# Kernel tuning notes

Measured on AMD Instinct MI355X. Metric: run time of the kernel, lower is better.

## Reference

```python
import jax, jax.numpy as jnp
import numpy as np

L = 10      # num_mp_layers
N = 10000   # nodes
E = 160000  # edges (avg degree 16)
H = 128     # hidden_dim

def setup_inputs() -> dict:
    key = jax.random.key(0)
    ks = list(jax.random.split(key, 32))
    it = iter(ks)
    def nrm(shape, scale=0.05):
        return jax.random.normal(next(it), shape, dtype=jnp.float32) * scale
    inp = {
        'x': jax.random.normal(next(it), (N, 7), dtype=jnp.float32),
        'edge_index': jax.random.randint(next(it), (2, E), 0, N),
        'edge_attr': jax.random.normal(next(it), (E, 8), dtype=jnp.float32),
        # encoder: Linear(7,H) + LayerNorm(H) (+GELU)
        'enc_W': nrm((7, H)), 'enc_b': jnp.zeros((H,), jnp.float32),
        'enc_g': jnp.ones((H,), jnp.float32), 'enc_beta': jnp.zeros((H,), jnp.float32),
        # edge encoder: Linear(8,H)
        'eenc_W': nrm((8, H)), 'eenc_b': jnp.zeros((H,), jnp.float32),
        # per-layer edge MLP: Linear(3H,2H)+LN+GELU+Linear(2H,H)+LN (stacked over L)
        'eW1': nrm((L, 3 * H, 2 * H)), 'eb1': jnp.zeros((L, 2 * H), jnp.float32),
        'eg1': jnp.ones((L, 2 * H), jnp.float32), 'ebt1': jnp.zeros((L, 2 * H), jnp.float32),
        'eW2': nrm((L, 2 * H, H)), 'eb2': jnp.zeros((L, H), jnp.float32),
        'eg2': jnp.ones((L, H), jnp.float32), 'ebt2': jnp.zeros((L, H), jnp.float32),
        # per-layer node MLP: Linear(2H,2H)+LN+GELU+Linear(2H,H)+LN (stacked over L)
        'nW1': nrm((L, 2 * H, 2 * H)), 'nb1': jnp.zeros((L, 2 * H), jnp.float32),
        'ng1': jnp.ones((L, 2 * H), jnp.float32), 'nbt1': jnp.zeros((L, 2 * H), jnp.float32),
        'nW2': nrm((L, 2 * H, H)), 'nb2': jnp.zeros((L, H), jnp.float32),
        'ng2': jnp.ones((L, H), jnp.float32), 'nbt2': jnp.zeros((L, H), jnp.float32),
        # decoder: Linear(H,H)+GELU+Linear(H,4)
        'dW1': nrm((H, H)), 'db1': jnp.zeros((H,), jnp.float32),
        'dW2': nrm((H, 4)), 'db2': jnp.zeros((4,), jnp.float32),
    }
    return inp

def _ln(h, g, b):
    m = jnp.mean(h, axis=-1, keepdims=True)
    v = jnp.var(h, axis=-1, keepdims=True)  # biased, matches torch LayerNorm
    return (h - m) * jax.lax.rsqrt(v + 1e-5) * g + b

def _mlp(h, W1, b1, g1, bt1, W2, b2, g2, bt2):
    # Linear -> LayerNorm -> GELU (exact erf) -> [Dropout=eval noop] -> Linear -> LayerNorm
    h = jax.nn.gelu(_ln(h @ W1 + b1, g1, bt1), approximate=False)
    return _ln(h @ W2 + b2, g2, bt2)

def reference(x, edge_index, edge_attr,
              enc_W, enc_b, enc_g, enc_beta, eenc_W, eenc_b,
              eW1, eb1, eg1, ebt1, eW2, eb2, eg2, ebt2,
              nW1, nb1, ng1, nbt1, nW2, nb2, ng2, nbt2,
              dW1, db1, dW2, db2):
    row, col = edge_index[0], edge_index[1]
    n_nodes = x.shape[0]
    h = jax.nn.gelu(_ln(x @ enc_W + enc_b, enc_g, enc_beta), approximate=False)  # [N,H]
    e = edge_attr @ eenc_W + eenc_b                                              # [E,H]

    def step(carry, p):
        h, e = carry
        (w1, b1, g1, bt1, w2, b2, g2, bt2,
         v1, c1, m1, mt1, v2, c2, m2, mt2) = p
        # edge update: gather -> concat -> MLP -> residual
        edge_in = jnp.concatenate([h[row], h[col], e], axis=1)       # [E,3H]
        e = e + _mlp(edge_in, w1, b1, g1, bt1, w2, b2, g2, bt2)
        # scatter-mean aggregation onto destination (col) nodes
        agg = jax.ops.segment_sum(e, col, num_segments=n_nodes)      # [N,H]
        cnt = jax.ops.segment_sum(jnp.ones((e.shape[0], 1), e.dtype), col,
                                  num_segments=n_nodes)
        agg = agg / jnp.maximum(cnt, 1.0)
        # node update: concat -> MLP -> residual
        node_in = jnp.concatenate([h, agg], axis=1)                  # [N,2H]
        h = h + _mlp(node_in, v1, c1, m1, mt1, v2, c2, m2, mt2)
        return (h, e), None

    layer_params = (eW1, eb1, eg1, ebt1, eW2, eb2, eg2, ebt2,
                    nW1, nb1, ng1, nbt1, nW2, nb2, ng2, nbt2)
    (h, e), _ = jax.lax.scan(step, (h, e), layer_params)
    out = jax.nn.gelu(h @ dW1 + db1, approximate=False) @ dW2 + db2  # [N,4]
    return out
```

## Files before the change

kernel.cpp:

```cpp
#include <hip/hip_runtime.h>

#define L_LAYERS 10
#define NN 10000
#define EE 160000

typedef unsigned short ushort_t;
typedef unsigned int uint_t;
typedef __attribute__((ext_vector_type(8))) short bf16x8;
typedef __attribute__((ext_vector_type(4))) float floatx4;

__device__ __forceinline__ ushort_t f2b(float f) {
  uint_t u = __float_as_uint(f);
  u += 0x7FFFu + ((u >> 16) & 1u);
  return (ushort_t)(u >> 16);
}
__device__ __forceinline__ float b2f(ushort_t v) {
  return __uint_as_float(((uint_t)v) << 16);
}
__device__ __forceinline__ uint_t pk2(float lo, float hi) {
  uint_t ul = __float_as_uint(lo), uh = __float_as_uint(hi);
  ul += 0x7FFFu + ((ul >> 16) & 1u);
  uh += 0x7FFFu + ((uh >> 16) & 1u);
  return (ul >> 16) | (uh & 0xFFFF0000u);
}
__device__ __forceinline__ float gelu_exact(float x) {
  return 0.5f * x * (1.0f + erff(x * 0.7071067811865475f));
}
__device__ __forceinline__ float gelu_fast(float x) {
  float x2 = x * x;
  float inner = fmaf(0.044715f * x2, x, x);
  float E = __expf(-1.5957691216f * inner);
  float R = __builtin_amdgcn_rcpf(1.0f + E);
  return x * R;
}
template <int CTRL>
__device__ __forceinline__ float dpp_addf(float x) {
  int y = __builtin_amdgcn_update_dpp(0, __float_as_int(x), CTRL, 0xF, 0xF, true);
  return x + __int_as_float(y);
}
__device__ __forceinline__ float row16_sum(float x) {
  x = dpp_addf<0xB1>(x);
  x = dpp_addf<0x4E>(x);
  x = dpp_addf<0x141>(x);
  x = dpp_addf<0x140>(x);
  return x;
}
#define MFMA16x32(a, b, c) __builtin_amdgcn_mfma_f32_16x16x32_bf16((a), (b), (c), 0, 0, 0)

__global__ __launch_bounds__(256) void k_pack_w(
    const float* __restrict__ W, ushort_t* __restrict__ P, int K, int N, int LKN)
{
  int idx = blockIdx.x * 256 + threadIdx.x;
  if (idx >= LKN) return;
  int n = idx % N;
  int t = idx / N;
  int k = t % K;
  int l = t / K;
  int ks = k >> 5, kk = k & 31;
  int Ks = K >> 5;
  P[(((size_t)((l * Ks + ks) * N + n)) << 5) + kk] = f2b(W[idx]);
}

__global__ __launch_bounds__(128) void k_encoder(
    const float* __restrict__ x, const float* __restrict__ W,
    const float* __restrict__ b, const float* __restrict__ g,
    const float* __restrict__ bt, float* __restrict__ h, ushort_t* __restrict__ h_bf)
{
  const int n = blockIdx.x;
  const int j = threadIdx.x;
  __shared__ float xs[7];
  __shared__ float red[4];
  if (j < 7) xs[j] = x[n * 7 + j];
  __syncthreads();
  float z = b[j];
  #pragma unroll
  for (int k = 0; k < 7; ++k) z = fmaf(xs[k], W[k * 128 + j], z);
  float sm = z, sq = z * z;
  #pragma unroll
  for (int off = 32; off > 0; off >>= 1) {
    sm += __shfl_down(sm, off);
    sq += __shfl_down(sq, off);
  }
  const int wv = j >> 6, ln = j & 63;
  if (ln == 0) { red[wv] = sm; red[2 + wv] = sq; }
  __syncthreads();
  float m = (red[0] + red[1]) * (1.0f / 128.0f);
  float var = (red[2] + red[3]) * (1.0f / 128.0f) - m * m;
  float zz = (z - m) * rsqrtf(var + 1e-5f) * g[j] + bt[j];
  float o = gelu_exact(zz);
  h[(size_t)n * 128 + j] = o;
  h_bf[(size_t)n * 128 + j] = f2b(o);
}

__global__ __launch_bounds__(256) void k_edge_enc(
    const float* __restrict__ ea, const float* __restrict__ W,
    const float* __restrict__ b, ushort_t* __restrict__ e_bf)
{
  const int i = blockIdx.x * 256 + threadIdx.x;
  const int eid = i >> 7, j = i & 127;
  float z = b[j];
  #pragma unroll
  for (int k = 0; k < 8; ++k) z = fmaf(ea[eid * 8 + k], W[k * 128 + j], z);
  e_bf[i] = f2b(z);
}

__global__ void k_zero_cnt(int* __restrict__ cnt) {
  int i = blockIdx.x * 256 + threadIdx.x;
  if (i < NN) cnt[i] = 0;
}
__global__ void k_count(const int* __restrict__ eidx, int* __restrict__ cnt) {
  int i = blockIdx.x * 256 + threadIdx.x;
  atomicAdd(&cnt[eidx[EE + i]], 1);
}
__global__ __launch_bounds__(256) void k_scan(
    const int* __restrict__ cnt, int* __restrict__ rowptr, int* __restrict__ fillp)
{
  __shared__ int tot[256];
  __shared__ int off[257];
  const int t = threadIdx.x;
  const int C = 40;
  int s = 0;
  int lo = t * C, hi = lo + C; if (hi > NN) hi = NN;
  for (int i = lo; i < hi; ++i) s += cnt[i];
  tot[t] = s;
  __syncthreads();
  if (t == 0) {
    int r = 0;
    for (int i = 0; i < 256; ++i) { off[i] = r; r += tot[i]; }
    off[256] = r;
  }
  __syncthreads();
  int r = off[t];
  for (int i = lo; i < hi; ++i) {
    rowptr[i] = r; fillp[i] = r;
    r += cnt[i];
  }
  if (t == 0) rowptr[NN] = off[256];
}
__global__ void k_fill(const int* __restrict__ eidx, int* __restrict__ fillp,
                       int* __restrict__ edge_of) {
  int i = blockIdx.x * 256 + threadIdx.x;
  int c = eidx[EE + i];
  int pos = atomicAdd(&fillp[c], 1);
  edge_of[pos] = i;
}

__global__ __launch_bounds__(512) void k_hpre(
    const ushort_t* __restrict__ h_bf, const ushort_t* __restrict__ W1pk,
    const float* __restrict__ b1, ushort_t* __restrict__ Hpre, int layer)
{
  __shared__ __align__(16) ushort_t A16[32 * 136];
  const int tid = threadIdx.x;
  const int base = blockIdx.x * 32;
  const ushort_t* W1p = W1pk + (size_t)layer * (12 * 256 * 32);
  const float* b1p = b1 + layer * 256;

  {
    const int ei = tid >> 4, c = tid & 15;
    const int g = base + ei;
    uint4 v = {0u, 0u, 0u, 0u};
    if (g < NN) v = *(const uint4*)(h_bf + (size_t)g * 128 + c * 8);
    *(uint4*)&A16[ei * 136 + c * 8] = v;
  }
  __syncthreads();

  const int lane = tid & 63;
  const int wv = tid >> 6;
  const int ln15 = lane & 15;
  const int quad = lane >> 4;

  const int g0 = wv * 64;
  const int ksb = (g0 < 256) ? 0 : 4;
  const int ncol = (g0 < 256) ? g0 : (g0 - 256);

  floatx4 acc[2][4];
  #pragma unroll
  for (int mi = 0; mi < 2; ++mi)
    #pragma unroll
    for (int ni = 0; ni < 4; ++ni) acc[mi][ni] = (floatx4){0.f, 0.f, 0.f, 0.f};

  for (int ks = 0; ks < 4; ++ks) {
    bf16x8 a0 = *(const bf16x8*)&A16[ln15 * 136 + ks * 32 + quad * 8];
    bf16x8 a1 = *(const bf16x8*)&A16[(16 + ln15) * 136 + ks * 32 + quad * 8];
    #pragma unroll
    for (int ni = 0; ni < 4; ++ni) {
      bf16x8 b = *(const bf16x8*)&W1p[((size_t)((ksb + ks) * 256 + ncol + ni * 16 + ln15) << 5) + quad * 8];
      acc[0][ni] = MFMA16x32(a0, b, acc[0][ni]);
      acc[1][ni] = MFMA16x32(a1, b, acc[1][ni]);
    }
  }

  float bbv[4];
  #pragma unroll
  for (int ni = 0; ni < 4; ++ni)
    bbv[ni] = (g0 < 256) ? b1p[ncol + ni * 16 + ln15] : 0.0f;

  #pragma unroll
  for (int mi = 0; mi < 2; ++mi)
    #pragma unroll
    for (int r = 0; r < 4; ++r) {
      int row = mi * 16 + quad * 4 + r;
      int g = base + row;
      if (g < NN) {
        float v0 = acc[mi][0][r] + bbv[0];
        float v1 = acc[mi][1][r] + bbv[1];
        float v2 = acc[mi][2][r] + bbv[2];
        float v3 = acc[mi][3][r] + bbv[3];
        uint2 pv;
        pv.x = pk2(v0, v1);
        pv.y = pk2(v2, v3);
        *(uint2*)&Hpre[(size_t)g * 512 + g0 + ln15 * 4] = pv;
      }
    }
}

__global__ __launch_bounds__(256) void k_edge_mlp_mfma(
    const ushort_t* __restrict__ Hpre, ushort_t* __restrict__ e_bf,
    const int* __restrict__ eidx,
    const ushort_t* __restrict__ W1pk, const ushort_t* __restrict__ W2pk,
    const float* __restrict__ g1, const float* __restrict__ bt1,
    const float* __restrict__ b2, const float* __restrict__ g2, const float* __restrict__ bt2,
    int layer)
{
  __shared__ __align__(16) ushort_t A16[32 * 136];
  __shared__ __align__(16) ushort_t Z16[32 * 264];
  __shared__ float red_s[32 * 4], red_q[32 * 4];
  __shared__ int s_row[32], s_col[32];

  const int tid = threadIdx.x;
  const int base = blockIdx.x * 32;
  const ushort_t* W1p = W1pk + (size_t)layer * (12 * 256 * 32);
  const ushort_t* W2p = W2pk + (size_t)layer * (8 * 128 * 32);
  const float* g1p = g1 + layer * 256;
  const float* bt1p = bt1 + layer * 256;
  const float* b2p = b2 + layer * 128;
  const float* g2p = g2 + layer * 128;
  const float* bt2p = bt2 + layer * 128;

  if (tid < 32) s_row[tid] = eidx[base + tid];
  else if (tid < 64) s_col[tid - 32] = eidx[EE + base + (tid - 32)];
  __syncthreads();

  #pragma unroll
  for (int i = 0; i < 2; ++i) {
    int idx = tid + i * 256;
    int ei = idx >> 4, c = idx & 15;
    *(uint4*)&A16[ei * 136 + c * 8] =
        *(const uint4*)(e_bf + (size_t)(base + ei) * 128 + c * 8);
  }
  __syncthreads();

  const int lane = tid & 63;
  const int wv = tid >> 6;
  const int ln15 = lane & 15;
  const int quad = lane >> 4;

  floatx4 acc[2][4];
  #pragma unroll
  for (int mi = 0; mi < 2; ++mi)
    #pragma unroll
    for (int ni = 0; ni < 4; ++ni) acc[mi][ni] = (floatx4){0.f, 0.f, 0.f, 0.f};

  const int nb1 = wv * 64;
  for (int ks = 0; ks < 4; ++ks) {
    bf16x8 a0 = *(const bf16x8*)&A16[ln15 * 136 + ks * 32 + quad * 8];
    bf16x8 a1 = *(const bf16x8*)&A16[(16 + ln15) * 136 + ks * 32 + quad * 8];
    #pragma unroll
    for (int ni = 0; ni < 4; ++ni) {
      bf16x8 b = *(const bf16x8*)&W1p[((size_t)((8 + ks) * 256 + nb1 + ni * 16 + ln15) << 5) + quad * 8];
      acc[0][ni] = MFMA16x32(a0, b, acc[0][ni]);
      acc[1][ni] = MFMA16x32(a1, b, acc[1][ni]);
    }
  }

  {
    const int po = nb1 + ln15 * 4;
    #pragma unroll
    for (int mi = 0; mi < 2; ++mi)
      #pragma unroll
      for (int r = 0; r < 4; ++r) {
        int row = mi * 16 + quad * 4 + r;
        uint2 vr = *(const uint2*)(Hpre + (size_t)s_row[row] * 512 + po);
        uint2 vc = *(const uint2*)(Hpre + (size_t)s_col[row] * 512 + 256 + po);
        acc[mi][0][r] += __uint_as_float(vr.x << 16) + __uint_as_float(vc.x << 16);
        acc[mi][1][r] += __uint_as_float(vr.x & 0xFFFF0000u) + __uint_as_float(vc.x & 0xFFFF0000u);
        acc[mi][2][r] += __uint_as_float(vr.y << 16) + __uint_as_float(vc.y << 16);
        acc[mi][3][r] += __uint_as_float(vr.y & 0xFFFF0000u) + __uint_as_float(vc.y & 0xFFFF0000u);
      }
  }

  #pragma unroll
  for (int mi = 0; mi < 2; ++mi)
    #pragma unroll
    for (int r = 0; r < 4; ++r) {
      float v = 0.f, u = 0.f;
      #pragma unroll
      for (int ni = 0; ni < 4; ++ni) { float x = acc[mi][ni][r]; v += x; u += x * x; }
      v = row16_sum(v); u = row16_sum(u);
      if (ln15 == 0) {
        int row = mi * 16 + quad * 4 + r;
        red_s[row * 4 + wv] = v; red_q[row * 4 + wv] = u;
      }
    }
  __syncthreads();

  float mrow[2][4], rrow[2][4];
  #pragma unroll
  for (int mi = 0; mi < 2; ++mi)
    #pragma unroll
    for (int r = 0; r < 4; ++r) {
      int row = mi * 16 + quad * 4 + r;
      float S = red_s[row * 4] + red_s[row * 4 + 1] + red_s[row * 4 + 2] + red_s[row * 4 + 3];
      float Q = red_q[row * 4] + red_q[row * 4 + 1] + red_q[row * 4 + 2] + red_q[row * 4 + 3];
      float m = S * (1.f / 256.f);
      float var = Q * (1.f / 256.f) - m * m;
      mrow[mi][r] = m; rrow[mi][r] = rsqrtf(var + 1e-5f);
    }
  #pragma unroll
  for (int ni = 0; ni < 4; ++ni) {
    int col = nb1 + ni * 16 + ln15;
    float gg = g1p[col], bb = bt1p[col];
    #pragma unroll
    for (int mi = 0; mi < 2; ++mi)
      #pragma unroll
      for (int r = 0; r < 4; ++r) {
        int row = mi * 16 + quad * 4 + r;
        float z = (acc[mi][ni][r] - mrow[mi][r]) * rrow[mi][r] * gg + bb;
        Z16[row * 264 + col] = f2b(gelu_fast(z));
      }
  }
  __syncthreads();

  floatx4 c2[2][2];
  #pragma unroll
  for (int mi = 0; mi < 2; ++mi)
    #pragma unroll
    for (int ni = 0; ni < 2; ++ni) c2[mi][ni] = (floatx4){0.f, 0.f, 0.f, 0.f};

  const int nb2 = wv * 32;
  {
    const ushort_t* Wf = W2p + ((size_t)(nb2 + ln15) << 5) + quad * 8;
    bf16x8 bA[2], bB[2];
    #pragma unroll
    for (int ni = 0; ni < 2; ++ni) bA[ni] = *(const bf16x8*)(Wf + (size_t)ni * (16 << 5));
    #pragma unroll
    for (int ks = 0; ks < 8; ks += 2) {
      #pragma unroll
      for (int ni = 0; ni < 2; ++ni)
        bB[ni] = *(const bf16x8*)(Wf + (size_t)(ks + 1) * (128 << 5) + (size_t)ni * (16 << 5));
      {
        bf16x8 a0 = *(const bf16x8*)&Z16[ln15 * 264 + ks * 32 + quad * 8];
        bf16x8 a1 = *(const bf16x8*)&Z16[(16 + ln15) * 264 + ks * 32 + quad * 8];
        #pragma unroll
        for (int ni = 0; ni < 2; ++ni) {
          c2[0][ni] = MFMA16x32(a0, bA[ni], c2[0][ni]);
          c2[1][ni] = MFMA16x32(a1, bA[ni], c2[1][ni]);
        }
      }
      if (ks + 2 < 8) {
        #pragma unroll
        for (int ni = 0; ni < 2; ++ni)
          bA[ni] = *(const bf16x8*)(Wf + (size_t)(ks + 2) * (128 << 5) + (size_t)ni * (16 << 5));
      }
      {
        bf16x8 a0 = *(const bf16x8*)&Z16[ln15 * 264 + (ks + 1) * 32 + quad * 8];
        bf16x8 a1 = *(const bf16x8*)&Z16[(16 + ln15) * 264 + (ks + 1) * 32 + quad * 8];
        #pragma unroll
        for (int ni = 0; ni < 2; ++ni) {
          c2[0][ni] = MFMA16x32(a0, bB[ni], c2[0][ni]);
          c2[1][ni] = MFMA16x32(a1, bB[ni], c2[1][ni]);
        }
      }
    }
  }

  #pragma unroll
  for (int ni = 0; ni < 2; ++ni) {
    float bb = b2p[nb2 + ni * 16 + ln15];
    #pragma unroll
    for (int mi = 0; mi < 2; ++mi)
      #pragma unroll
      for (int r = 0; r < 4; ++r) c2[mi][ni][r] += bb;
  }
  #pragma unroll
  for (int mi = 0; mi < 2; ++mi)
    #pragma unroll
    for (int r = 0; r < 4; ++r) {
      float v = 0.f, u = 0.f;
      #pragma unroll
      for (int ni = 0; ni < 2; ++ni) { float x = c2[mi][ni][r]; v += x; u += x * x; }
      v = row16_sum(v); u = row16_sum(u);
      if (ln15 == 0) {
        int row = mi * 16 + quad * 4 + r;
        red_s[row * 4 + wv] = v; red_q[row * 4 + wv] = u;
      }
    }
  __syncthreads();

  #pragma unroll
  for (int mi = 0; mi < 2; ++mi)
    #pragma unroll
    for (int r = 0; r < 4; ++r) {
      int row = mi * 16 + quad * 4 + r;
      float S = red_s[row * 4] + red_s[row * 4 + 1] + red_s[row * 4 + 2] + red_s[row * 4 + 3];
      float Q = red_q[row * 4] + red_q[row * 4 + 1] + red_q[row * 4 + 2] + red_q[row * 4 + 3];
      float m = S * (1.f / 128.f);
      float var = Q * (1.f / 128.f) - m * m;
      mrow[mi][r] = m; rrow[mi][r] = rsqrtf(var + 1e-5f);
    }
  #pragma unroll
  for (int ni = 0; ni < 2; ++ni) {
    int col = nb2 + ni * 16 + ln15;
    float gg = g2p[col], bb = bt2p[col];
    #pragma unroll
    for (int mi = 0; mi < 2; ++mi)
      #pragma unroll
      for (int r = 0; r < 4; ++r) {
        int row = mi * 16 + quad * 4 + r;
        float z = (c2[mi][ni][r] - mrow[mi][r]) * rrow[mi][r] * gg + bb;
        size_t gi = (size_t)(base + row) * 128 + col;
        e_bf[gi] = f2b(b2f(e_bf[gi]) + z);
      }
  }
}

__global__ __launch_bounds__(256) void k_node_mlp_mfma(
    float* __restrict__ h, ushort_t* __restrict__ h_bf, const ushort_t* __restrict__ e_bf,
    const int* __restrict__ rowptr, const int* __restrict__ edge_of,
    const ushort_t* __restrict__ W1pk, const ushort_t* __restrict__ W2pk,
    const float* __restrict__ b1, const float* __restrict__ g1, const float* __restrict__ bt1,
    const float* __restrict__ b2, const float* __restrict__ g2, const float* __restrict__ bt2,
    int layer)
{
  __shared__ __align__(16) ushort_t A16[32 * 264];
  __shared__ float red_s[32 * 4], red_q[32 * 4];
  ushort_t* Z16 = A16;

  const int tid = threadIdx.x;
  const int base = blockIdx.x * 32;
  const ushort_t* W1p = W1pk + (size_t)layer * (8 * 256 * 32);
  const ushort_t* W2p = W2pk + (size_t)layer * (8 * 128 * 32);
  const float* b1p = b1 + layer * 256;
  const float* g1p = g1 + layer * 256;
  const float* bt1p = bt1 + layer * 256;
  const float* b2p = b2 + layer * 128;
  const float* g2p = g2 + layer * 128;
  const float* bt2p = bt2 + layer * 128;

  {
    const int node = tid >> 3, seg = tid & 7;
    const int g = base + node;
    if (g < NN) {
      *(uint4*)&A16[node * 264 + seg * 16] =
          *(const uint4*)(h_bf + (size_t)g * 128 + seg * 16);
      *(uint4*)&A16[node * 264 + seg * 16 + 8] =
          *(const uint4*)(h_bf + (size_t)g * 128 + seg * 16 + 8);
      const int s = rowptr[g], en = rowptr[g + 1];
      float a[16];
      #pragma unroll
      for (int q = 0; q < 16; ++q) a[q] = 0.f;
      for (int it = s; it < en; ++it) {
        const ushort_t* src = e_bf + (size_t)edge_of[it] * 128 + seg * 16;
        uint4 v0 = *(const uint4*)src;
        uint4 v1 = *(const uint4*)(src + 8);
        a[0] += __uint_as_float(v0.x << 16); a[1] += __uint_as_float(v0.x & 0xFFFF0000u);
        a[2] += __uint_as_float(v0.y << 16); a[3] += __uint_as_float(v0.y & 0xFFFF0000u);
        a[4] += __uint_as_float(v0.z << 16); a[5] += __uint_as_float(v0.z & 0xFFFF0000u);
        a[6] += __uint_as_float(v0.w << 16); a[7] += __uint_as_float(v0.w & 0xFFFF0000u);
        a[8]  += __uint_as_float(v1.x << 16); a[9]  += __uint_as_float(v1.x & 0xFFFF0000u);
        a[10] += __uint_as_float(v1.y << 16); a[11] += __uint_as_float(v1.y & 0xFFFF0000u);
        a[12] += __uint_as_float(v1.z << 16); a[13] += __uint_as_float(v1.z & 0xFFFF0000u);
        a[14] += __uint_as_float(v1.w << 16); a[15] += __uint_as_float(v1.w & 0xFFFF0000u);
      }
      int c = en - s;
      float inv = 1.0f / (float)(c > 0 ? c : 1);
      uint4 p0, p1;
      p0.x = pk2(a[0] * inv, a[1] * inv);  p0.y = pk2(a[2] * inv, a[3] * inv);
      p0.z = pk2(a[4] * inv, a[5] * inv);  p0.w = pk2(a[6] * inv, a[7] * inv);
      p1.x = pk2(a[8] * inv, a[9] * inv);  p1.y = pk2(a[10] * inv, a[11] * inv);
      p1.z = pk2(a[12] * inv, a[13] * inv); p1.w = pk2(a[14] * inv, a[15] * inv);
      *(uint4*)&A16[node * 264 + 128 + seg * 16] = p0;
      *(uint4*)&A16[node * 264 + 128 + seg * 16 + 8] = p1;
    } else {
      uint4 zz = {0u, 0u, 0u, 0u};
      *(uint4*)&A16[node * 264 + seg * 16] = zz;
      *(uint4*)&A16[node * 264 + seg * 16 + 8] = zz;
      *(uint4*)&A16[node * 264 + 128 + seg * 16] = zz;
      *(uint4*)&A16[node * 264 + 128 + seg * 16 + 8] = zz;
    }
  }
  __syncthreads();

  const int lane = tid & 63;
  const int wv = tid >> 6;
  const int ln15 = lane & 15;
  const int quad = lane >> 4;

  floatx4 acc[2][4];
  #pragma unroll
  for (int mi = 0; mi < 2; ++mi)
    #pragma unroll
    for (int ni = 0; ni < 4; ++ni) acc[mi][ni] = (floatx4){0.f, 0.f, 0.f, 0.f};

  const int nb1 = wv * 64;
  for (int ks = 0; ks < 8; ++ks) {
    bf16x8 a0 = *(const bf16x8*)&A16[ln15 * 264 + ks * 32 + quad * 8];
    bf16x8 a1 = *(const bf16x8*)&A16[(16 + ln15) * 264 + ks * 32 + quad * 8];
    #pragma unroll
    for (int ni = 0; ni < 4; ++ni) {
      bf16x8 b = *(const bf16x8*)&W1p[((size_t)(ks * 256 + nb1 + ni * 16 + ln15) << 5) + quad * 8];
      acc[0][ni] = MFMA16x32(a0, b, acc[0][ni]);
      acc[1][ni] = MFMA16x32(a1, b, acc[1][ni]);
    }
  }

  #pragma unroll
  for (int ni = 0; ni < 4; ++ni) {
    float bb = b1p[nb1 + ni * 16 + ln15];
    #pragma unroll
    for (int mi = 0; mi < 2; ++mi)
      #pragma unroll
      for (int r = 0; r < 4; ++r) acc[mi][ni][r] += bb;
  }
  #pragma unroll
  for (int mi = 0; mi < 2; ++mi)
    #pragma unroll
    for (int r = 0; r < 4; ++r) {
      float v = 0.f, u = 0.f;
      #pragma unroll
      for (int ni = 0; ni < 4; ++ni) { float x = acc[mi][ni][r]; v += x; u += x * x; }
      v = row16_sum(v); u = row16_sum(u);
      if (ln15 == 0) {
        int row = mi * 16 + quad * 4 + r;
        red_s[row * 4 + wv] = v; red_q[row * 4 + wv] = u;
      }
    }
  __syncthreads();

  float mrow[2][4], rrow[2][4];
  #pragma unroll
  for (int mi = 0; mi < 2; ++mi)
    #pragma unroll
    for (int r = 0; r < 4; ++r) {
      int row = mi * 16 + quad * 4 + r;
      float S = red_s[row * 4] + red_s[row * 4 + 1] + red_s[row * 4 + 2] + red_s[row * 4 + 3];
      float Q = red_q[row * 4] + red_q[row * 4 + 1] + red_q[row * 4 + 2] + red_q[row * 4 + 3];
      float m = S * (1.f / 256.f);
      float var = Q * (1.f / 256.f) - m * m;
      mrow[mi][r] = m; rrow[mi][r] = rsqrtf(var + 1e-5f);
    }
  #pragma unroll
  for (int ni = 0; ni < 4; ++ni) {
    int col = nb1 + ni * 16 + ln15;
    float gg = g1p[col], bb = bt1p[col];
    #pragma unroll
    for (int mi = 0; mi < 2; ++mi)
      #pragma unroll
      for (int r = 0; r < 4; ++r) {
        int row = mi * 16 + quad * 4 + r;
        float z = (acc[mi][ni][r] - mrow[mi][r]) * rrow[mi][r] * gg + bb;
        Z16[row * 264 + col] = f2b(gelu_fast(z));
      }
  }
  __syncthreads();

  floatx4 c2[2][2];
  #pragma unroll
  for (int mi = 0; mi < 2; ++mi)
    #pragma unroll
    for (int ni = 0; ni < 2; ++ni) c2[mi][ni] = (floatx4){0.f, 0.f, 0.f, 0.f};

  const int nb2 = wv * 32;
  for (int ks = 0; ks < 8; ++ks) {
    bf16x8 a0 = *(const bf16x8*)&Z16[ln15 * 264 + ks * 32 + quad * 8];
    bf16x8 a1 = *(const bf16x8*)&Z16[(16 + ln15) * 264 + ks * 32 + quad * 8];
    #pragma unroll
    for (int ni = 0; ni < 2; ++ni) {
      bf16x8 b = *(const bf16x8*)&W2p[((size_t)(ks * 128 + nb2 + ni * 16 + ln15) << 5) + quad * 8];
      c2[0][ni] = MFMA16x32(a0, b, c2[0][ni]);
      c2[1][ni] = MFMA16x32(a1, b, c2[1][ni]);
    }
  }

  #pragma unroll
  for (int ni = 0; ni < 2; ++ni) {
    float bb = b2p[nb2 + ni * 16 + ln15];
    #pragma unroll
    for (int mi = 0; mi < 2; ++mi)
      #pragma unroll
      for (int r = 0; r < 4; ++r) c2[mi][ni][r] += bb;
  }
  #pragma unroll
  for (int mi = 0; mi < 2; ++mi)
    #pragma unroll
    for (int r = 0; r < 4; ++r) {
      float v = 0.f, u = 0.f;
      #pragma unroll
      for (int ni = 0; ni < 2; ++ni) { float x = c2[mi][ni][r]; v += x; u += x * x; }
      v = row16_sum(v); u = row16_sum(u);
      if (ln15 == 0) {
        int row = mi * 16 + quad * 4 + r;
        red_s[row * 4 + wv] = v; red_q[row * 4 + wv] = u;
      }
    }
  __syncthreads();

  #pragma unroll
  for (int mi = 0; mi < 2; ++mi)
    #pragma unroll
    for (int r = 0; r < 4; ++r) {
      int row = mi * 16 + quad * 4 + r;
      float S = red_s[row * 4] + red_s[row * 4 + 1] + red_s[row * 4 + 2] + red_s[row * 4 + 3];
      float Q = red_q[row * 4] + red_q[row * 4 + 1] + red_q[row * 4 + 2] + red_q[row * 4 + 3];
      float m = S * (1.f / 128.f);
      float var = Q * (1.f / 128.f) - m * m;
      mrow[mi][r] = m; rrow[mi][r] = rsqrtf(var + 1e-5f);
    }
  #pragma unroll
  for (int ni = 0; ni < 2; ++ni) {
    int col = nb2 + ni * 16 + ln15;
    float gg = g2p[col], bb = bt2p[col];
    #pragma unroll
    for (int mi = 0; mi < 2; ++mi)
      #pragma unroll
      for (int r = 0; r < 4; ++r) {
        int row = mi * 16 + quad * 4 + r;
        int g = base + row;
        if (g < NN) {
          float z = (c2[mi][ni][r] - mrow[mi][r]) * rrow[mi][r] * gg + bb;
          size_t gi = (size_t)g * 128 + col;
          float nv = h[gi] + z;
          h[gi] = nv;
          h_bf[gi] = f2b(nv);
        }
      }
  }
}

__global__ __launch_bounds__(128) void k_decoder(
    const float* __restrict__ h, const float* __restrict__ W1,
    const float* __restrict__ b1, const float* __restrict__ W2,
    const float* __restrict__ b2, float* __restrict__ out)
{
  const int n = blockIdx.x;
  const int j = threadIdx.x;
  __shared__ float hs[128];
  __shared__ float z1s[128];
  hs[j] = h[(size_t)n * 128 + j];
  __syncthreads();
  float z = b1[j];
  for (int k = 0; k < 128; ++k) z = fmaf(hs[k], W1[k * 128 + j], z);
  z1s[j] = gelu_exact(z);
  __syncthreads();
  if (j < 4) {
    float o = b2[j];
    for (int k = 0; k < 128; ++k) o = fmaf(z1s[k], W2[k * 4 + j], o);
    out[n * 4 + j] = o;
  }
}

static inline char* align_up(char* p, size_t a) {
  return (char*)(((uintptr_t)p + (a - 1)) & ~(uintptr_t)(a - 1));
}

extern "C" void kernel_launch(void* const* d_in, const int* in_sizes, int n_in,
                              void* d_out, int out_size, void* d_ws, size_t ws_size,
                              hipStream_t stream) {
  const float* x     = (const float*)d_in[0];
  const int*   eidx  = (const int*)d_in[1];
  const float* ea    = (const float*)d_in[2];
  const float* encW  = (const float*)d_in[3];
  const float* encb  = (const float*)d_in[4];
  const float* encg  = (const float*)d_in[5];
  const float* encbt = (const float*)d_in[6];
  const float* eencW = (const float*)d_in[7];
  const float* eencb = (const float*)d_in[8];
  const float* eW1   = (const float*)d_in[9];
  const float* eb1   = (const float*)d_in[10];
  const float* eg1   = (const float*)d_in[11];
  const float* ebt1  = (const float*)d_in[12];
  const float* eW2   = (const float*)d_in[13];
  const float* eb2   = (const float*)d_in[14];
  const float* eg2   = (const float*)d_in[15];
  const float* ebt2  = (const float*)d_in[16];
  const float* nW1   = (const float*)d_in[17];
  const float* nb1   = (const float*)d_in[18];
  const float* ng1   = (const float*)d_in[19];
  const float* nbt1  = (const float*)d_in[20];
  const float* nW2   = (const float*)d_in[21];
  const float* nb2   = (const float*)d_in[22];
  const float* ng2   = (const float*)d_in[23];
  const float* nbt2  = (const float*)d_in[24];
  const float* dW1   = (const float*)d_in[25];
  const float* db1   = (const float*)d_in[26];
  const float* dW2   = (const float*)d_in[27];
  const float* db2   = (const float*)d_in[28];
  float* out = (float*)d_out;

  char* p = (char*)d_ws;
  float* h   = (float*)p; p += (size_t)NN * 128 * 4;
  int* cnt     = (int*)p; p += (size_t)NN * 4;
  int* rowptr  = (int*)p; p += (size_t)(NN + 1) * 4;
  int* fillp   = (int*)p; p += (size_t)NN * 4;
  int* edge_of = (int*)p; p += (size_t)EE * 4;
  p = align_up(p, 256);
  ushort_t* h_bf = (ushort_t*)p; p += (size_t)NN * 128 * 2;
  p = align_up(p, 256);
  ushort_t* e_bf = (ushort_t*)p; p += (size_t)EE * 128 * 2;
  p = align_up(p, 256);
  ushort_t* Hpre = (ushort_t*)p; p += (size_t)NN * 512 * 2;
  p = align_up(p, 256);
  ushort_t* eW1pk = (ushort_t*)p; p += (size_t)L_LAYERS * 12 * 256 * 32 * 2;
  p = align_up(p, 256);
  ushort_t* eW2pk = (ushort_t*)p; p += (size_t)L_LAYERS * 8 * 128 * 32 * 2;
  p = align_up(p, 256);
  ushort_t* nW1pk = (ushort_t*)p; p += (size_t)L_LAYERS * 8 * 256 * 32 * 2;
  p = align_up(p, 256);
  ushort_t* nW2pk = (ushort_t*)p; p += (size_t)L_LAYERS * 8 * 128 * 32 * 2;

  {
    int n1 = L_LAYERS * 384 * 256;
    k_pack_w<<<(n1 + 255) / 256, 256, 0, stream>>>(eW1, eW1pk, 384, 256, n1);
    int n2 = L_LAYERS * 256 * 128;
    k_pack_w<<<(n2 + 255) / 256, 256, 0, stream>>>(eW2, eW2pk, 256, 128, n2);
    int n3 = L_LAYERS * 256 * 256;
    k_pack_w<<<(n3 + 255) / 256, 256, 0, stream>>>(nW1, nW1pk, 256, 256, n3);
    int n4 = L_LAYERS * 256 * 128;
    k_pack_w<<<(n4 + 255) / 256, 256, 0, stream>>>(nW2, nW2pk, 256, 128, n4);
  }

  k_encoder<<<NN, 128, 0, stream>>>(x, encW, encb, encg, encbt, h, h_bf);
  k_edge_enc<<<(EE * 128) / 256, 256, 0, stream>>>(ea, eencW, eencb, e_bf);
  k_zero_cnt<<<(NN + 255) / 256, 256, 0, stream>>>(cnt);
  k_count<<<EE / 256, 256, 0, stream>>>(eidx, cnt);
  k_scan<<<1, 256, 0, stream>>>(cnt, rowptr, fillp);
  k_fill<<<EE / 256, 256, 0, stream>>>(eidx, fillp, edge_of);

  for (int l = 0; l < L_LAYERS; ++l) {
    k_hpre<<<(NN + 31) / 32, 512, 0, stream>>>(h_bf, eW1pk, eb1, Hpre, l);
    k_edge_mlp_mfma<<<EE / 32, 256, 0, stream>>>(Hpre, e_bf, eidx,
        eW1pk, eW2pk, eg1, ebt1, eb2, eg2, ebt2, l);
    k_node_mlp_mfma<<<(NN + 31) / 32, 256, 0, stream>>>(h, h_bf, e_bf, rowptr, edge_of,
        nW1pk, nW2pk, nb1, ng1, nbt1, nb2, ng2, nbt2, l);
  }
  k_decoder<<<NN, 128, 0, stream>>>(h, dW1, db1, dW2, db2, out);
}
```

Measured before the change: 1.458 ms.

## Fuse next-layer Hpre projection into node MLP kernel epilogue

The node MLP kernel now writes the updated bf16 node features into shared memory and then computes the next layer's per-node projection (Hpre) with MFMA, using the first two K-blocks of the edge W1. This removes the separate k_hpre launch for layers 1..9, along with its re-read of h_bf. Only the initial layer still runs k_hpre. The trade-off is extra register and compute work at the tail of the node kernel, with possible occupancy pressure.

```diff
diff --git a/kernel.cpp b/kernel.cpp
--- a/kernel.cpp
+++ b/kernel.cpp
@@ -430,7 +430,8 @@
     const ushort_t* __restrict__ W1pk, const ushort_t* __restrict__ W2pk,
     const float* __restrict__ b1, const float* __restrict__ g1, const float* __restrict__ bt1,
     const float* __restrict__ b2, const float* __restrict__ g2, const float* __restrict__ bt2,
-    int layer)
+    const ushort_t* __restrict__ eW1pk, const float* __restrict__ eb1,
+    ushort_t* __restrict__ Hpre, int layer, int hl)
 {
   __shared__ __align__(16) ushort_t A16[32 * 264];
   __shared__ float red_s[32 * 4], red_q[32 * 4];
@@ -626,14 +627,60 @@
       for (int r = 0; r < 4; ++r) {
         int row = mi * 16 + quad * 4 + r;
         int g = base + row;
+        float nv = 0.f;
         if (g < NN) {
           float z = (c2[mi][ni][r] - mrow[mi][r]) * rrow[mi][r] * gg + bb;
           size_t gi = (size_t)g * 128 + col;
-          float nv = h[gi] + z;
+          nv = h[gi] + z;
           h[gi] = nv;
           h_bf[gi] = f2b(nv);
         }
-      }
+        Z16[row * 264 + col] = f2b(nv);
+      }
+  }
+
+  if (hl >= 0) {
+    __syncthreads();
+    const ushort_t* hW1p = eW1pk + (size_t)hl * (12 * 256 * 32);
+    const float* hb1p = eb1 + hl * 256;
+    const int ncol = wv * 64;
+    #pragma unroll
+    for (int blk = 0; blk < 2; ++blk) {
+      const int ksb = blk ? 4 : 0;
+      const int g0 = blk ? (256 + ncol) : ncol;
+      floatx4 ah[2][4];
+      #pragma unroll
+      for (int mi = 0; mi < 2; ++mi)
+        #pragma unroll
+        for (int ni = 0; ni < 4; ++ni) ah[mi][ni] = (floatx4){0.f, 0.f, 0.f, 0.f};
+      for (int ks = 0; ks < 4; ++ks) {
+        bf16x8 a0 = *(const bf16x8*)&Z16[ln15 * 264 + ks * 32 + quad * 8];
+        bf16x8 a1 = *(const bf16x8*)&Z16[(16 + ln15) * 264 + ks * 32 + quad * 8];
+        #pragma unroll
+        for (int ni = 0; ni < 4; ++ni) {
+          bf16x8 b = *(const bf16x8*)&hW1p[((size_t)((ksb + ks) * 256 + ncol + ni * 16 + ln15) << 5) + quad * 8];
+          ah[0][ni] = MFMA16x32(a0, b, ah[0][ni]);
+          ah[1][ni] = MFMA16x32(a1, b, ah[1][ni]);
+        }
+      }
+      float bbv[4];
+      #pragma unroll
+      for (int ni = 0; ni < 4; ++ni)
+        bbv[ni] = blk ? 0.0f : hb1p[ncol + ni * 16 + ln15];
+      #pragma unroll
+      for (int mi = 0; mi < 2; ++mi)
+        #pragma unroll
+        for (int r = 0; r < 4; ++r) {
+          int row = mi * 16 + quad * 4 + r;
+          int g = base + row;
+          if (g < NN) {
+            uint2 pv;
+            pv.x = pk2(ah[mi][0][r] + bbv[0], ah[mi][1][r] + bbv[1]);
+            pv.y = pk2(ah[mi][2][r] + bbv[2], ah[mi][3][r] + bbv[3]);
+            *(uint2*)&Hpre[(size_t)g * 512 + g0 + ln15 * 4] = pv;
+          }
+        }
+    }
   }
 }
 
@@ -736,12 +783,15 @@
   k_scan<<<1, 256, 0, stream>>>(cnt, rowptr, fillp);
   k_fill<<<EE / 256, 256, 0, stream>>>(eidx, fillp, edge_of);
 
+  k_hpre<<<(NN + 31) / 32, 512, 0, stream>>>(h_bf, eW1pk, eb1, Hpre, 0);
+
   for (int l = 0; l < L_LAYERS; ++l) {
-    k_hpre<<<(NN + 31) / 32, 512, 0, stream>>>(h_bf, eW1pk, eb1, Hpre, l);
     k_edge_mlp_mfma<<<EE / 32, 256, 0, stream>>>(Hpre, e_bf, eidx,
         eW1pk, eW2pk, eg1, ebt1, eb2, eg2, ebt2, l);
+    int hl = (l + 1 < L_LAYERS) ? (l + 1) : -1;
     k_node_mlp_mfma<<<(NN + 31) / 32, 256, 0, stream>>>(h, h_bf, e_bf, rowptr, edge_of,
-        nW1pk, nW2pk, nb1, ng1, nbt1, nb2, ng2, nbt2, l);
+        nW1pk, nW2pk, nb1, ng1, nbt1, nb2, ng2, nbt2,
+        eW1pk, eb1, Hpre, l, hl);
   }
   k_decoder<<<NN, 128, 0, stream>>>(h, dW1, db1, dW2, db2, out);
 }
```

Measured after the change: 1.438 ms. Within noise of the previous version (-1.3%).
